# Optimization experiments

Hardware: AMD Instinct MI355X
Metric: run time of the kernel (lower is better)

Reference implementation:

```python
import jax, jax.numpy as jnp
import numpy as np

# Static graph layout: B equal-size graphs so per-graph topk has a fixed size.
NUM_GRAPHS = 512
NODES_PER_GRAPH = 256
K_PER_GRAPH = 128  # ceil(0.5 * NODES_PER_GRAPH), ratio = 0.5
NUM_EDGES = 4_194_304  # avg degree 32
D_FEAT = 128
D_EDGE = 16


def setup_inputs() -> dict:
    key = jax.random.key(0)
    k1, k2, k3, k4, k5, k6 = jax.random.split(key, 6)
    N = NUM_GRAPHS * NODES_PER_GRAPH
    x = jax.random.normal(k1, (N, D_FEAT), dtype=jnp.float32)
    # Edges are sampled within a graph (realistic PyG batched-graph structure).
    g = jax.random.randint(k2, (NUM_EDGES,), 0, NUM_GRAPHS)
    src = g * NODES_PER_GRAPH + jax.random.randint(k3, (NUM_EDGES,), 0, NODES_PER_GRAPH)
    dst = g * NODES_PER_GRAPH + jax.random.randint(k4, (NUM_EDGES,), 0, NODES_PER_GRAPH)
    edge_index = jnp.stack([src, dst]).astype(jnp.int32)
    edge_attr = jax.random.normal(k5, (NUM_EDGES, D_EDGE), dtype=jnp.float32)
    batch = jnp.repeat(jnp.arange(NUM_GRAPHS, dtype=jnp.int32), NODES_PER_GRAPH)
    W = jax.random.normal(k6, (D_FEAT,), dtype=jnp.float32) / np.sqrt(D_FEAT)
    b = jnp.zeros((1,), dtype=jnp.float32)
    return {"x": x, "edge_index": edge_index, "edge_attr": edge_attr,
            "batch": batch, "W": W, "b": b}


def reference(x, edge_index, edge_attr, batch, W, b):
    N, D = x.shape
    B, n, k = NUM_GRAPHS, NODES_PER_GRAPH, K_PER_GRAPH
    K = B * k

    # --- SelectSparse: linear scoring (Linear(in_channels, 1)) ---
    scores = x @ W + b[0]                      # [N]
    # Per-graph top-k (batch is sorted with equal-size graphs -> reshape).
    top_vals, top_idx = jax.lax.top_k(scores.reshape(B, n), k)  # [B, k]
    perm = (top_idx + (jnp.arange(B) * n)[:, None]).reshape(-1)  # [K] global ids
    w = top_vals.reshape(-1)                   # scores[perm], descending per graph

    # --- gather + scale selected node features ---
    x_out = x[perm] * w[:, None]               # [K, D]

    # --- FilterEdges: keep edges with both endpoints selected, remap ids ---
    node_map = jnp.full((N,), -1, dtype=jnp.int32).at[perm].set(
        jnp.arange(K, dtype=jnp.int32))
    new_src = node_map[edge_index[0]]
    new_dst = node_map[edge_index[1]]
    mask = (new_src >= 0) & (new_dst >= 0)
    # Stable-compaction of kept edges to the front; tail padded with -1 / 0
    # (fixed output shape in lieu of torch's dynamic-shape edge filtering).
    order = jnp.argsort(jnp.logical_not(mask), stable=True)
    kept = mask[order]
    new_ei = jnp.stack([new_src[order], new_dst[order]])
    new_ei = jnp.where(kept[None, :], new_ei, -1)   # [2, E]
    new_attr = jnp.where(kept[:, None], edge_attr[order], 0.0)  # [E, D_EDGE]
    new_batch = batch[perm]                    # [K]

    return x_out, new_ei, new_attr, new_batch, perm, w
```

## Files before the change

kernel.cpp:

```cpp
#include <hip/hip_runtime.h>

#define NGRAPH 512
#define NPG    256
#define KPG    128
#define NN     (NGRAPH * NPG)
#define KK     (NGRAPH * KPG)
#define NE     4194304
#define DF     128
#define DE     16

#define SBLK   256
#define EPB    1024
#define NTILE  (NE / EPB)

typedef float vf4 __attribute__((ext_vector_type(4)));

#define OUT_X     0ull
#define OUT_EI    ((size_t)KK * DF)
#define OUT_ATTR  (OUT_EI + 2ull * NE)
#define OUT_BATCH (OUT_ATTR + (size_t)NE * DE)
#define OUT_PERM  (OUT_BATCH + KK)
#define OUT_W     (OUT_PERM + KK)

__global__ void score_kernel(const float* __restrict__ x,
                             const float* __restrict__ W,
                             const float* __restrict__ b,
                             float* __restrict__ scores) {
    int t = threadIdx.x;
    int l32 = t & 31;
    int node = blockIdx.x * 8 + (t >> 5);
    float4 xv = ((const float4*)(x + (size_t)node * DF))[l32];
    float4 wv = ((const float4*)W)[l32];
    float s = xv.x * wv.x + xv.y * wv.y + xv.z * wv.z + xv.w * wv.w;
    #pragma unroll
    for (int off = 16; off > 0; off >>= 1) s += __shfl_down(s, off, 32);
    if (l32 == 0) scores[node] = s + b[0];
}

__global__ void __launch_bounds__(NPG)
topk_gather_kernel(const float* __restrict__ scores,
                   const float* __restrict__ x,
                   int* __restrict__ node_map,
                   unsigned* __restrict__ nkbits,
                   float* __restrict__ out) {
    __shared__ float s[NPG];
    __shared__ int   sel[KPG];
    __shared__ float selw[KPG];
    int g = blockIdx.x, t = threadIdx.x;
    int wave = t >> 6, lane = t & 63;
    float my = scores[g * NPG + t];
    s[t] = my;
    __syncthreads();
    int rank = 0;
    #pragma unroll 8
    for (int j = 0; j < NPG; j++) {
        float o = s[j];
        rank += (o > my) || (o == my && j < t);
    }
    bool kept = rank < KPG;
    if (kept) {
        int node = g * NPG + t;
        int nid  = g * KPG + rank;
        node_map[node] = nid;
        sel[rank]  = t;
        selw[rank] = my;
        out[OUT_BATCH + nid] = (float)g;
        out[OUT_PERM + nid]  = (float)node;
        out[OUT_W + nid]     = my;
    }
    unsigned long long bal = __ballot(kept);
    if (lane == 0)  nkbits[g * 8 + wave * 2]     = (unsigned)bal;
    if (lane == 32) nkbits[g * 8 + wave * 2 + 1] = (unsigned)(bal >> 32);
    __syncthreads();
    int l32 = t & 31, rsub = t >> 5;
    #pragma unroll
    for (int it = 0; it < KPG / 8; it++) {
        int r = it * 8 + rsub;
        int node = g * NPG + sel[r];
        float wv = selw[r];
        float4 v = ((const float4*)(x + (size_t)node * DF))[l32];
        v.x *= wv; v.y *= wv; v.z *= wv; v.w *= wv;
        ((float4*)(out + OUT_X + ((size_t)g * KPG + r) * DF))[l32] = v;
    }
}

__global__ void __launch_bounds__(SBLK)
mapstage_kernel(const int* __restrict__ ei,
                const int* __restrict__ node_map,
                const unsigned* __restrict__ nkbits,
                unsigned* __restrict__ pk_ws,
                unsigned short* __restrict__ kl_ws,
                int* __restrict__ tilecounts) {
    int tile = blockIdx.x, t = threadIdx.x;
    int wave = t >> 6, lane = t & 63;
    __shared__ int wtot[4];

    int ebase = tile * EPB + t * 4;
    int4 sv = *(const int4*)(ei + ebase);
    int4 dv = *(const int4*)(ei + NE + ebase);
    #define KB(n) ((nkbits[(unsigned)(n) >> 5] >> ((unsigned)(n) & 31u)) & 1u)
    unsigned bits = (KB(sv.x) & KB(dv.x))
                  | ((KB(sv.y) & KB(dv.y)) << 1)
                  | ((KB(sv.z) & KB(dv.z)) << 2)
                  | ((KB(sv.w) & KB(dv.w)) << 3);
    #undef KB
    int c = __popc(bits);
    int inc = c;
    #pragma unroll
    for (int off = 1; off < 64; off <<= 1) {
        int u = __shfl_up(inc, off, 64);
        if (lane >= off) inc += u;
    }
    if (lane == 63) wtot[wave] = inc;
    __syncthreads();
    int wbase = 0;
    #pragma unroll
    for (int i = 0; i < 4; i++) if (i < wave) wbase += wtot[i];
    int pre = wbase + inc - c;

    if (bits) {
        int s4[4] = {sv.x, sv.y, sv.z, sv.w};
        int d4[4] = {dv.x, dv.y, dv.z, dv.w};
        #pragma unroll
        for (int j = 0; j < 4; j++) {
            if ((bits >> j) & 1u) {
                unsigned ns = (unsigned)node_map[s4[j]];
                unsigned nd = (unsigned)node_map[d4[j]];
                pk_ws[tile * EPB + pre] = (ns << 16) | nd;
                kl_ws[tile * EPB + pre] = (unsigned short)(t * 4 + j);
                pre++;
            }
        }
    }
    if (t == 0) tilecounts[tile] = wtot[0] + wtot[1] + wtot[2] + wtot[3];
}

__global__ void __launch_bounds__(256)
scan_kernel(const int* __restrict__ tilecounts,
            int* __restrict__ tileoffs) {
    const int PER = NTILE / 256;
    int t = threadIdx.x;
    int base = t * PER;
    int s = 0;
    #pragma unroll
    for (int j = 0; j < PER; j++) s += tilecounts[base + j];
    __shared__ int ls[256];
    ls[t] = s;
    __syncthreads();
    for (int off = 1; off < 256; off <<= 1) {
        int v = (t >= off) ? ls[t - off] : 0;
        __syncthreads();
        ls[t] += v;
        __syncthreads();
    }
    int run = ls[t] - s;
    #pragma unroll
    for (int j = 0; j < PER; j++) {
        int c = tilecounts[base + j];
        tileoffs[base + j] = run;
        run += c;
    }
}

__global__ void __launch_bounds__(SBLK)
scatter_kernel(const float* __restrict__ eattr,
               const unsigned* __restrict__ pk_ws,
               const unsigned short* __restrict__ kl_ws,
               const int* __restrict__ tilecounts,
               const int* __restrict__ tileoffs,
               float* __restrict__ out) {
    int tile = blockIdx.x, t = threadIdx.x;
    int cnt  = tilecounts[tile];
    int excl = tileoffs[tile];

    for (int j = t; j < cnt; j += SBLK) {
        unsigned p = pk_ws[tile * EPB + j];
        __builtin_nontemporal_store((float)(p >> 16),     &out[OUT_EI + excl + j]);
        __builtin_nontemporal_store((float)(p & 0xFFFFu), &out[OUT_EI + NE + excl + j]);
    }
    int sub = t & 3;
    for (int j = t >> 2; j < cnt; j += SBLK / 4) {
        int el = kl_ws[tile * EPB + j];
        const vf4* sp = (const vf4*)(eattr + ((size_t)tile * EPB + el) * DE);
        vf4 v = __builtin_nontemporal_load(sp + sub);
        vf4* dp = (vf4*)(out + OUT_ATTR + ((size_t)excl + j) * DE);
        __builtin_nontemporal_store(v, dp + sub);
    }
    int disc_excl = tile * EPB - excl;
    int disc = EPB - cnt;
    size_t tail_lo = (size_t)NE - disc_excl - disc;
    for (int i = t; i < disc; i += SBLK) {
        __builtin_nontemporal_store(-1.f, &out[OUT_EI + tail_lo + i]);
        __builtin_nontemporal_store(-1.f, &out[OUT_EI + NE + tail_lo + i]);
    }
    vf4* ap = (vf4*)(out + OUT_ATTR);
    vf4 z = (vf4){0.f, 0.f, 0.f, 0.f};
    for (int i = t; i < disc * 4; i += SBLK)
        __builtin_nontemporal_store(z, &ap[tail_lo * 4 + i]);
}

extern "C" void kernel_launch(void* const* d_in, const int* in_sizes, int n_in,
                              void* d_out, int out_size, void* d_ws, size_t ws_size,
                              hipStream_t stream) {
    const float* x     = (const float*)d_in[0];
    const int*   ei    = (const int*)d_in[1];
    const float* eattr = (const float*)d_in[2];
    const float* W     = (const float*)d_in[4];
    const float* b     = (const float*)d_in[5];
    float* out = (float*)d_out;

    float*          scores     = (float*)d_ws;
    int*            node_map   = (int*)(scores + NN);
    unsigned*       nkbits     = (unsigned*)(node_map + NN);
    int*            tilecounts = (int*)(nkbits + NN / 32);
    int*            tileoffs   = tilecounts + NTILE;
    unsigned*       pk_ws      = (unsigned*)(tileoffs + NTILE);
    unsigned short* kl_ws      = (unsigned short*)(pk_ws + NE);

    score_kernel      <<<NN / 8, 256, 0, stream>>>(x, W, b, scores);
    topk_gather_kernel<<<NGRAPH, NPG, 0, stream>>>(scores, x, node_map, nkbits, out);
    mapstage_kernel   <<<NTILE, SBLK, 0, stream>>>(ei, node_map, nkbits, pk_ws, kl_ws, tilecounts);
    scan_kernel       <<<1, 256, 0, stream>>>(tilecounts, tileoffs);
    scatter_kernel    <<<NTILE, SBLK, 0, stream>>>(eattr, pk_ws, kl_ws, tilecounts, tileoffs, out);
}
```

Measured before the change: 151.8 us.

## Fuse scoring into top-k kernel and fold tile scan into scatter

Scoring is computed inside the per-graph top-k block, so the separate score kernel and its scores buffer round trip go away. The single-block scan kernel is removed, and each scatter block instead sums all preceding tile counts itself to get its offset. This saves two launches and a serialized scan. In exchange each scatter block does redundant O(tile) reads of tilecounts (up to 4096). Nontemporal loads and stores are also added for the edge-index reads and the x_out writes.

```diff
diff --git a/kernel.cpp b/kernel.cpp
--- a/kernel.cpp
+++ b/kernel.cpp
@@ -14,6 +14,7 @@
 #define NTILE  (NE / EPB)
 
 typedef float vf4 __attribute__((ext_vector_type(4)));
+typedef int   vi4 __attribute__((ext_vector_type(4)));
 
 #define OUT_X     0ull
 #define OUT_EI    ((size_t)KK * DF)
@@ -22,35 +23,33 @@
 #define OUT_PERM  (OUT_BATCH + KK)
 #define OUT_W     (OUT_PERM + KK)
 
-__global__ void score_kernel(const float* __restrict__ x,
-                             const float* __restrict__ W,
-                             const float* __restrict__ b,
-                             float* __restrict__ scores) {
-    int t = threadIdx.x;
-    int l32 = t & 31;
-    int node = blockIdx.x * 8 + (t >> 5);
-    float4 xv = ((const float4*)(x + (size_t)node * DF))[l32];
-    float4 wv = ((const float4*)W)[l32];
-    float s = xv.x * wv.x + xv.y * wv.y + xv.z * wv.z + xv.w * wv.w;
-    #pragma unroll
-    for (int off = 16; off > 0; off >>= 1) s += __shfl_down(s, off, 32);
-    if (l32 == 0) scores[node] = s + b[0];
-}
-
 __global__ void __launch_bounds__(NPG)
-topk_gather_kernel(const float* __restrict__ scores,
-                   const float* __restrict__ x,
-                   int* __restrict__ node_map,
-                   unsigned* __restrict__ nkbits,
-                   float* __restrict__ out) {
+topk_all_kernel(const float* __restrict__ x,
+                const float* __restrict__ W,
+                const float* __restrict__ b,
+                int* __restrict__ node_map,
+                unsigned* __restrict__ nkbits,
+                float* __restrict__ out) {
     __shared__ float s[NPG];
     __shared__ int   sel[KPG];
     __shared__ float selw[KPG];
     int g = blockIdx.x, t = threadIdx.x;
     int wave = t >> 6, lane = t & 63;
-    float my = scores[g * NPG + t];
-    s[t] = my;
-    __syncthreads();
+    int l32 = t & 31, grp = t >> 5;
+    float bias = b[0];
+
+    float4 wv = ((const float4*)W)[l32];
+    #pragma unroll 4
+    for (int it = 0; it < NPG / 8; it++) {
+        int r = it * 8 + grp;
+        float4 xv = ((const float4*)(x + ((size_t)g * NPG + r) * DF))[l32];
+        float sum = xv.x * wv.x + xv.y * wv.y + xv.z * wv.z + xv.w * wv.w;
+        #pragma unroll
+        for (int off = 16; off > 0; off >>= 1) sum += __shfl_down(sum, off, 32);
+        if (l32 == 0) s[r] = sum + bias;
+    }
+    __syncthreads();
+    float my = s[t];
     int rank = 0;
     #pragma unroll 8
     for (int j = 0; j < NPG; j++) {
@@ -72,15 +71,16 @@
     if (lane == 0)  nkbits[g * 8 + wave * 2]     = (unsigned)bal;
     if (lane == 32) nkbits[g * 8 + wave * 2 + 1] = (unsigned)(bal >> 32);
     __syncthreads();
-    int l32 = t & 31, rsub = t >> 5;
     #pragma unroll
     for (int it = 0; it < KPG / 8; it++) {
-        int r = it * 8 + rsub;
+        int r = it * 8 + grp;
         int node = g * NPG + sel[r];
-        float wv = selw[r];
-        float4 v = ((const float4*)(x + (size_t)node * DF))[l32];
-        v.x *= wv; v.y *= wv; v.z *= wv; v.w *= wv;
-        ((float4*)(out + OUT_X + ((size_t)g * KPG + r) * DF))[l32] = v;
+        float wvs = selw[r];
+        const vf4* sp = (const vf4*)(x + (size_t)node * DF);
+        vf4 v = sp[l32];
+        v *= wvs;
+        __builtin_nontemporal_store(v,
+            (vf4*)(out + OUT_X + ((size_t)g * KPG + r) * DF) + l32);
     }
 }
 
@@ -96,8 +96,8 @@
     __shared__ int wtot[4];
 
     int ebase = tile * EPB + t * 4;
-    int4 sv = *(const int4*)(ei + ebase);
-    int4 dv = *(const int4*)(ei + NE + ebase);
+    vi4 sv = __builtin_nontemporal_load((const vi4*)(ei + ebase));
+    vi4 dv = __builtin_nontemporal_load((const vi4*)(ei + NE + ebase));
     #define KB(n) ((nkbits[(unsigned)(n) >> 5] >> ((unsigned)(n) & 31u)) & 1u)
     unsigned bits = (KB(sv.x) & KB(dv.x))
                   | ((KB(sv.y) & KB(dv.y)) << 1)
@@ -135,43 +135,27 @@
     if (t == 0) tilecounts[tile] = wtot[0] + wtot[1] + wtot[2] + wtot[3];
 }
 
-__global__ void __launch_bounds__(256)
-scan_kernel(const int* __restrict__ tilecounts,
-            int* __restrict__ tileoffs) {
-    const int PER = NTILE / 256;
-    int t = threadIdx.x;
-    int base = t * PER;
-    int s = 0;
-    #pragma unroll
-    for (int j = 0; j < PER; j++) s += tilecounts[base + j];
-    __shared__ int ls[256];
-    ls[t] = s;
-    __syncthreads();
-    for (int off = 1; off < 256; off <<= 1) {
-        int v = (t >= off) ? ls[t - off] : 0;
-        __syncthreads();
-        ls[t] += v;
-        __syncthreads();
-    }
-    int run = ls[t] - s;
-    #pragma unroll
-    for (int j = 0; j < PER; j++) {
-        int c = tilecounts[base + j];
-        tileoffs[base + j] = run;
-        run += c;
-    }
-}
-
 __global__ void __launch_bounds__(SBLK)
 scatter_kernel(const float* __restrict__ eattr,
                const unsigned* __restrict__ pk_ws,
                const unsigned short* __restrict__ kl_ws,
                const int* __restrict__ tilecounts,
-               const int* __restrict__ tileoffs,
                float* __restrict__ out) {
     int tile = blockIdx.x, t = threadIdx.x;
+    int wave = t >> 6, lane = t & 63;
+    __shared__ int warr[4];
+    __shared__ int s_excl;
+
+    int partial = 0;
+    for (int i = t; i < tile; i += SBLK) partial += tilecounts[i];
+    #pragma unroll
+    for (int off = 32; off > 0; off >>= 1) partial += __shfl_down(partial, off, 64);
+    if (lane == 0) warr[wave] = partial;
+    __syncthreads();
+    if (t == 0) s_excl = warr[0] + warr[1] + warr[2] + warr[3];
+    __syncthreads();
+    int excl = s_excl;
     int cnt  = tilecounts[tile];
-    int excl = tileoffs[tile];
 
     for (int j = t; j < cnt; j += SBLK) {
         unsigned p = pk_ws[tile * EPB + j];
@@ -209,17 +193,13 @@
     const float* b     = (const float*)d_in[5];
     float* out = (float*)d_out;
 
-    float*          scores     = (float*)d_ws;
-    int*            node_map   = (int*)(scores + NN);
+    int*            node_map   = (int*)d_ws;
     unsigned*       nkbits     = (unsigned*)(node_map + NN);
     int*            tilecounts = (int*)(nkbits + NN / 32);
-    int*            tileoffs   = tilecounts + NTILE;
-    unsigned*       pk_ws      = (unsigned*)(tileoffs + NTILE);
+    unsigned*       pk_ws      = (unsigned*)(tilecounts + NTILE);
     unsigned short* kl_ws      = (unsigned short*)(pk_ws + NE);
 
-    score_kernel      <<<NN / 8, 256, 0, stream>>>(x, W, b, scores);
-    topk_gather_kernel<<<NGRAPH, NPG, 0, stream>>>(scores, x, node_map, nkbits, out);
-    mapstage_kernel   <<<NTILE, SBLK, 0, stream>>>(ei, node_map, nkbits, pk_ws, kl_ws, tilecounts);
-    scan_kernel       <<<1, 256, 0, stream>>>(tilecounts, tileoffs);
-    scatter_kernel    <<<NTILE, SBLK, 0, stream>>>(eattr, pk_ws, kl_ws, tilecounts, tileoffs, out);
-}
+    topk_all_kernel<<<NGRAPH, NPG, 0, stream>>>(x, W, b, node_map, nkbits, out);
+    mapstage_kernel<<<NTILE, SBLK, 0, stream>>>(ei, node_map, nkbits, pk_ws, kl_ws, tilecounts);
+    scatter_kernel <<<NTILE, SBLK, 0, stream>>>(eattr, pk_ws, kl_ws, tilecounts, out);
+}
```

Measured after the change: 151.2 us. No clear change (-0.4%).
